# Kernel tuning notes

Measured on AMD Instinct MI355X. Metric: run time of the kernel, lower is better.

## Reference

```python
import jax, jax.numpy as jnp
import numpy as np

NUM_UNITS = 64
IN_FEATURES = 256
OUT_FEATURES = 256


def _uw(x, w):
    # per-unit linear: x [B,U,I], w [U,I,O] -> [B,U,O]
    return jnp.einsum('bui,uio->buo', x, w)


def setup_inputs() -> dict:
    key = jax.random.key(0)
    ks = jax.random.split(key, 8)
    bound = float(np.sqrt(1.0 / OUT_FEATURES))
    U, I, O = NUM_UNITS, IN_FEATURES, OUT_FEATURES
    B = 256
    uni = lambda k, s: jax.random.uniform(k, s, jnp.float32, -bound, bound)
    return {
        'x': jax.random.normal(ks[0], (B, U, I), jnp.float32),
        'w_ir': uni(ks[1], (U, I, O)),
        'w_iz': uni(ks[2], (U, I, O)),
        'w_in': uni(ks[3], (U, I, O)),
        'w_hr': uni(ks[4], (U, O, O)),
        'w_hz': uni(ks[5], (U, O, O)),
        'w_hn': uni(ks[6], (U, O, O)),
        'hidden_init': uni(ks[7], (1, U, O)),
    }


def reference(x, w_ir, w_iz, w_in, w_hr, w_hz, w_hn, hidden_init):
    # hidden initialized by broadcasting hidden_init over batch (first call)
    h = jnp.broadcast_to(hidden_init, (x.shape[0],) + hidden_init.shape[1:])
    r = jax.nn.sigmoid(_uw(x, w_ir) + _uw(h, w_hr))
    z = jax.nn.sigmoid(_uw(x, w_iz) + _uw(h, w_hz))
    n = jnp.tanh(_uw(x, w_in) + r * _uw(h, w_hn))
    return (1.0 - z) * n + z * h
```

## Files before the change

kernel.cpp:

```cpp
#include <hip/hip_runtime.h>

#define BATCH 256
#define UNITS 64
#define IFEAT 256
#define OFEAT 256

typedef __attribute__((ext_vector_type(8))) short v8s;
typedef __attribute__((ext_vector_type(4))) float v4f;

static __device__ __forceinline__ unsigned short f2bf(float f) {
    unsigned int x = __float_as_uint(f);
    unsigned int r = x + 0x7fffu + ((x >> 16) & 1u);
    return (unsigned short)(r >> 16);
}

static __device__ __forceinline__ float sigmoid_f(float x) {
    return 1.0f / (1.0f + __expf(-x));
}
static __device__ __forceinline__ float tanh_f(float x) {
    float ax = fabsf(x);
    float e = __expf(-2.0f * ax);
    float t = (1.0f - e) / (1.0f + e);
    return copysignf(t, x);
}

__global__ void gru_hvec(const float* __restrict__ whr,
                         const float* __restrict__ whz,
                         const float* __restrict__ whn,
                         const float* __restrict__ hinit,
                         float* __restrict__ hv) {
    __shared__ float red[256];
    const int bid  = blockIdx.x;
    const int half = bid & 1;
    const int u    = (bid >> 1) & 63;
    const int w    = bid >> 7;
    const float* wh = (w == 0) ? whr : (w == 1) ? whz : whn;

    const int t = threadIdx.x;
    const int o = half * 128 + (t & 127);
    const int c = t >> 7;
    const float* hp = hinit + u * IFEAT;
    const float* wp = wh + (size_t)u * IFEAT * OFEAT + o;

    float acc = 0.0f;
    const int i0 = c * 128;
#pragma unroll 8
    for (int i = 0; i < 128; ++i) {
        acc += hp[i0 + i] * wp[(size_t)(i0 + i) * OFEAT];
    }
    red[t] = acc;
    __syncthreads();
    if (c == 0) hv[((size_t)w * UNITS + u) * OFEAT + o] = red[t] + red[t + 128];
}

__global__ __launch_bounds__(256, 3) void gru_gemm(
    const float* __restrict__ x,
    const float* __restrict__ wir,
    const float* __restrict__ wiz,
    const float* __restrict__ win,
    const float* __restrict__ hinit,
    const float* __restrict__ hv,
    float* __restrict__ out) {
    __shared__ unsigned short As[2][4][64][8];
    __shared__ unsigned short Bs[2][3][4][64][8];

    const int bid = blockIdx.x;
    const int u   = (bid & 7) + 8 * ((bid >> 3) >> 4);
    const int rem = (bid >> 3) & 15;
    const int b0  = (rem >> 2) * 64;
    const int o0  = (rem & 3) * 64;

    const int t    = threadIdx.x;
    const int lane = t & 63;
    const int wave = t >> 6;
    const int wm   = wave >> 1;
    const int wn   = wave & 1;
    const int lg   = lane >> 4;
    const int lr   = lane & 15;

    const int srow = t & 63;
    const int skg  = t >> 6;

    const size_t a_gbase = (size_t)(b0 + srow) * (UNITS * IFEAT)
                         + (size_t)u * IFEAT + skg * 8;
    const size_t b_gbase = (size_t)u * (IFEAT * OFEAT)
                         + (size_t)(skg * 8) * OFEAT + o0 + srow;

    v4f ra0, ra1;
    float rb0[8], rb1[8], rb2[8];

    auto stage_load = [&](int kk) {
        const float* ap = x + a_gbase + kk * 32;
        ra0 = *(const v4f*)ap;
        ra1 = *(const v4f*)(ap + 4);
        const size_t bo = b_gbase + (size_t)kk * 32 * OFEAT;
#pragma unroll
        for (int j = 0; j < 8; ++j) rb0[j] = wir[bo + (size_t)j * OFEAT];
#pragma unroll
        for (int j = 0; j < 8; ++j) rb1[j] = wiz[bo + (size_t)j * OFEAT];
#pragma unroll
        for (int j = 0; j < 8; ++j) rb2[j] = win[bo + (size_t)j * OFEAT];
    };

    auto stage_write = [&](int bb) {
        v8s av;
        av[0] = (short)f2bf(ra0[0]); av[1] = (short)f2bf(ra0[1]);
        av[2] = (short)f2bf(ra0[2]); av[3] = (short)f2bf(ra0[3]);
        av[4] = (short)f2bf(ra1[0]); av[5] = (short)f2bf(ra1[1]);
        av[6] = (short)f2bf(ra1[2]); av[7] = (short)f2bf(ra1[3]);
        *(v8s*)&As[bb][skg][srow][0] = av;
        v8s bv0, bv1, bv2;
#pragma unroll
        for (int j = 0; j < 8; ++j) bv0[j] = (short)f2bf(rb0[j]);
#pragma unroll
        for (int j = 0; j < 8; ++j) bv1[j] = (short)f2bf(rb1[j]);
#pragma unroll
        for (int j = 0; j < 8; ++j) bv2[j] = (short)f2bf(rb2[j]);
        *(v8s*)&Bs[bb][0][skg][srow][0] = bv0;
        *(v8s*)&Bs[bb][1][skg][srow][0] = bv1;
        *(v8s*)&Bs[bb][2][skg][srow][0] = bv2;
    };

    v4f acc[3][2][2];
#pragma unroll
    for (int g = 0; g < 3; ++g)
#pragma unroll
        for (int mi = 0; mi < 2; ++mi)
#pragma unroll
            for (int ni = 0; ni < 2; ++ni)
                acc[g][mi][ni] = (v4f){0.f, 0.f, 0.f, 0.f};

    stage_load(0);
    stage_write(0);
    stage_load(1);
    __syncthreads();

#pragma unroll 2
    for (int kk = 0; kk < 8; ++kk) {
        const int bb = kk & 1;
        if (kk < 7) stage_write(bb ^ 1);
        if (kk < 6) stage_load(kk + 2);

        v8s a0 = *(const v8s*)&As[bb][lg][wm * 32 + lr][0];
        v8s a1 = *(const v8s*)&As[bb][lg][wm * 32 + 16 + lr][0];
#pragma unroll
        for (int g = 0; g < 3; ++g) {
#pragma unroll
            for (int ni = 0; ni < 2; ++ni) {
                v8s b = *(const v8s*)&Bs[bb][g][lg][wn * 32 + ni * 16 + lr][0];
                acc[g][0][ni] = __builtin_amdgcn_mfma_f32_16x16x32_bf16(a0, b, acc[g][0][ni], 0, 0, 0);
                acc[g][1][ni] = __builtin_amdgcn_mfma_f32_16x16x32_bf16(a1, b, acc[g][1][ni], 0, 0, 0);
            }
        }
        if (kk < 7) __syncthreads();
    }

    const int obase = o0 + wn * 32 + lr;
    float hrv[2], hzv[2], hnv[2], h0v[2];
#pragma unroll
    for (int ni = 0; ni < 2; ++ni) {
        const int o = obase + ni * 16;
        hrv[ni] = hv[(0 * UNITS + u) * OFEAT + o];
        hzv[ni] = hv[(1 * UNITS + u) * OFEAT + o];
        hnv[ni] = hv[(2 * UNITS + u) * OFEAT + o];
        h0v[ni] = hinit[u * OFEAT + o];
    }
    const int rbase = b0 + wm * 32 + lg * 4;
#pragma unroll
    for (int mi = 0; mi < 2; ++mi) {
#pragma unroll
        for (int ni = 0; ni < 2; ++ni) {
            const int o = obase + ni * 16;
#pragma unroll
            for (int jj = 0; jj < 4; ++jj) {
                const int row = rbase + mi * 16 + jj;
                const float r = sigmoid_f(acc[0][mi][ni][jj] + hrv[ni]);
                const float z = sigmoid_f(acc[1][mi][ni][jj] + hzv[ni]);
                const float n = tanh_f(acc[2][mi][ni][jj] + r * hnv[ni]);
                out[((size_t)row * UNITS + u) * OFEAT + o] = (1.0f - z) * n + z * h0v[ni];
            }
        }
    }
}

extern "C" void kernel_launch(void* const* d_in, const int* in_sizes, int n_in,
                              void* d_out, int out_size, void* d_ws, size_t ws_size,
                              hipStream_t stream) {
    const float* x     = (const float*)d_in[0];
    const float* w_ir  = (const float*)d_in[1];
    const float* w_iz  = (const float*)d_in[2];
    const float* w_in  = (const float*)d_in[3];
    const float* w_hr  = (const float*)d_in[4];
    const float* w_hz  = (const float*)d_in[5];
    const float* w_hn  = (const float*)d_in[6];
    const float* hinit = (const float*)d_in[7];
    float* out = (float*)d_out;
    float* hv  = (float*)d_ws;

    gru_hvec<<<dim3(384), dim3(256), 0, stream>>>(w_hr, w_hz, w_hn, hinit, hv);
    gru_gemm<<<dim3(1024), dim3(256), 0, stream>>>(x, w_ir, w_iz, w_in, hinit, hv, out);
}
```

Before: 36.98 us.

## Halve GEMM output tile width and split hvec reduction four ways

The main GEMM now uses a 64x32 output tile per block instead of 64x64. That doubles the grid to 2048 blocks, halves the accumulator registers, and redistributes B-tile loads across threads, with the launch bound raised to 6 blocks per SM. The hidden-vector kernel runs 512 threads, each doing a quarter of the K reduction, for more parallelism. The risk is that each x tile is now loaded and converted twice, once per output half, which adds redundant A traffic and bf16 conversion.

Measured after the change: 43.34 us. +17.2%, slower.

```diff
diff --git a/kernel.cpp b/kernel.cpp
--- a/kernel.cpp
+++ b/kernel.cpp
@@ -24,12 +24,13 @@
     return copysignf(t, x);
 }
 
-__global__ void gru_hvec(const float* __restrict__ whr,
-                         const float* __restrict__ whz,
-                         const float* __restrict__ whn,
-                         const float* __restrict__ hinit,
-                         float* __restrict__ hv) {
-    __shared__ float red[256];
+__global__ __launch_bounds__(512, 8) void gru_hvec(
+        const float* __restrict__ whr,
+        const float* __restrict__ whz,
+        const float* __restrict__ whn,
+        const float* __restrict__ hinit,
+        float* __restrict__ hv) {
+    __shared__ float red[512];
     const int bid  = blockIdx.x;
     const int half = bid & 1;
     const int u    = (bid >> 1) & 63;
@@ -43,17 +44,19 @@
     const float* wp = wh + (size_t)u * IFEAT * OFEAT + o;
 
     float acc = 0.0f;
-    const int i0 = c * 128;
+    const int i0 = c * 64;
 #pragma unroll 8
-    for (int i = 0; i < 128; ++i) {
+    for (int i = 0; i < 64; ++i) {
         acc += hp[i0 + i] * wp[(size_t)(i0 + i) * OFEAT];
     }
     red[t] = acc;
     __syncthreads();
-    if (c == 0) hv[((size_t)w * UNITS + u) * OFEAT + o] = red[t] + red[t + 128];
+    if (c == 0)
+        hv[((size_t)w * UNITS + u) * OFEAT + o] =
+            red[t] + red[t + 128] + red[t + 256] + red[t + 384];
 }
 
-__global__ __launch_bounds__(256, 3) void gru_gemm(
+__global__ __launch_bounds__(256, 6) void gru_gemm(
     const float* __restrict__ x,
     const float* __restrict__ wir,
     const float* __restrict__ wiz,
@@ -62,13 +65,13 @@
     const float* __restrict__ hv,
     float* __restrict__ out) {
     __shared__ unsigned short As[2][4][64][8];
-    __shared__ unsigned short Bs[2][3][4][64][8];
+    __shared__ unsigned short Bs[2][3][4][32][8];
 
     const int bid = blockIdx.x;
-    const int u   = (bid & 7) + 8 * ((bid >> 3) >> 4);
-    const int rem = (bid >> 3) & 15;
-    const int b0  = (rem >> 2) * 64;
-    const int o0  = (rem & 3) * 64;
+    const int u   = (bid & 7) + 8 * (bid >> 8);
+    const int rem = (bid >> 3) & 31;
+    const int b0  = (rem >> 3) * 64;
+    const int o0  = (rem & 7) * 32;
 
     const int t    = threadIdx.x;
     const int lane = t & 63;
@@ -78,28 +81,34 @@
     const int lg   = lane >> 4;
     const int lr   = lane & 15;
 
-    const int srow = t & 63;
-    const int skg  = t >> 6;
+    const int arow = t & 63;
+    const int akg  = t >> 6;
+    const int a_gbase = (b0 + arow) * (UNITS * IFEAT) + u * IFEAT + akg * 8;
 
-    const size_t a_gbase = (size_t)(b0 + srow) * (UNITS * IFEAT)
-                         + (size_t)u * IFEAT + skg * 8;
-    const size_t b_gbase = (size_t)u * (IFEAT * OFEAT)
-                         + (size_t)(skg * 8) * OFEAT + o0 + srow;
+    const int it0 = t;
+    const int c0  = it0 & 31, kg0 = (it0 >> 5) & 3, g0 = it0 >> 7;
+    const float* wp0 = (g0 == 0) ? wir : wiz;
+    const bool has1 = (t < 128);
+    const int it1 = 256 + t;
+    const int c1  = it1 & 31, kg1 = (it1 >> 5) & 3;
+    const int bg0 = u * (IFEAT * OFEAT) + (kg0 * 8) * OFEAT + o0 + c0;
+    const int bg1 = u * (IFEAT * OFEAT) + (kg1 * 8) * OFEAT + o0 + c1;
 
     v4f ra0, ra1;
-    float rb0[8], rb1[8], rb2[8];
+    float rb0[8], rb1[8];
 
     auto stage_load = [&](int kk) {
         const float* ap = x + a_gbase + kk * 32;
         ra0 = *(const v4f*)ap;
         ra1 = *(const v4f*)(ap + 4);
-        const size_t bo = b_gbase + (size_t)kk * 32 * OFEAT;
+        const int off0 = bg0 + kk * 32 * OFEAT;
 #pragma unroll
-        for (int j = 0; j < 8; ++j) rb0[j] = wir[bo + (size_t)j * OFEAT];
+        for (int j = 0; j < 8; ++j) rb0[j] = wp0[off0 + j * OFEAT];
+        if (has1) {
+            const int off1 = bg1 + kk * 32 * OFEAT;
 #pragma unroll
-        for (int j = 0; j < 8; ++j) rb1[j] = wiz[bo + (size_t)j * OFEAT];
-#pragma unroll
-        for (int j = 0; j < 8; ++j) rb2[j] = win[bo + (size_t)j * OFEAT];
+            for (int j = 0; j < 8; ++j) rb1[j] = win[off1 + j * OFEAT];
+        }
     };
 
     auto stage_write = [&](int bb) {
@@ -108,27 +117,25 @@
         av[2] = (short)f2bf(ra0[2]); av[3] = (short)f2bf(ra0[3]);
         av[4] = (short)f2bf(ra1[0]); av[5] = (short)f2bf(ra1[1]);
         av[6] = (short)f2bf(ra1[2]); av[7] = (short)f2bf(ra1[3]);
-        *(v8s*)&As[bb][skg][srow][0] = av;
-        v8s bv0, bv1, bv2;
+        *(v8s*)&As[bb][akg][arow][0] = av;
+        v8s bv0;
 #pragma unroll
         for (int j = 0; j < 8; ++j) bv0[j] = (short)f2bf(rb0[j]);
+        *(v8s*)&Bs[bb][g0][kg0][c0][0] = bv0;
+        if (has1) {
+            v8s bv1;
 #pragma unroll
-        for (int j = 0; j < 8; ++j) bv1[j] = (short)f2bf(rb1[j]);
-#pragma unroll
-        for (int j = 0; j < 8; ++j) bv2[j] = (short)f2bf(rb2[j]);
-        *(v8s*)&Bs[bb][0][skg][srow][0] = bv0;
-        *(v8s*)&Bs[bb][1][skg][srow][0] = bv1;
-        *(v8s*)&Bs[bb][2][skg][srow][0] = bv2;
+            for (int j = 0; j < 8; ++j) bv1[j] = (short)f2bf(rb1[j]);
+            *(v8s*)&Bs[bb][2][kg1][c1][0] = bv1;
+        }
     };
 
-    v4f acc[3][2][2];
+    v4f acc[3][2];
 #pragma unroll
     for (int g = 0; g < 3; ++g)
 #pragma unroll
         for (int mi = 0; mi < 2; ++mi)
-#pragma unroll
-            for (int ni = 0; ni < 2; ++ni)
-                acc[g][mi][ni] = (v4f){0.f, 0.f, 0.f, 0.f};
+            acc[g][mi] = (v4f){0.f, 0.f, 0.f, 0.f};
 
     stage_load(0);
     stage_write(0);
@@ -145,40 +152,28 @@
         v8s a1 = *(const v8s*)&As[bb][lg][wm * 32 + 16 + lr][0];
 #pragma unroll
         for (int g = 0; g < 3; ++g) {
-#pragma unroll
-            for (int ni = 0; ni < 2; ++ni) {
-                v8s b = *(const v8s*)&Bs[bb][g][lg][wn * 32 + ni * 16 + lr][0];
-                acc[g][0][ni] = __builtin_amdgcn_mfma_f32_16x16x32_bf16(a0, b, acc[g][0][ni], 0, 0, 0);
-                acc[g][1][ni] = __builtin_amdgcn_mfma_f32_16x16x32_bf16(a1, b, acc[g][1][ni], 0, 0, 0);
-            }
+            v8s b = *(const v8s*)&Bs[bb][g][lg][wn * 16 + lr][0];
+            acc[g][0] = __builtin_amdgcn_mfma_f32_16x16x32_bf16(a0, b, acc[g][0], 0, 0, 0);
+            acc[g][1] = __builtin_amdgcn_mfma_f32_16x16x32_bf16(a1, b, acc[g][1], 0, 0, 0);
         }
         if (kk < 7) __syncthreads();
     }
 
-    const int obase = o0 + wn * 32 + lr;
-    float hrv[2], hzv[2], hnv[2], h0v[2];
-#pragma unroll
-    for (int ni = 0; ni < 2; ++ni) {
-        const int o = obase + ni * 16;
-        hrv[ni] = hv[(0 * UNITS + u) * OFEAT + o];
-        hzv[ni] = hv[(1 * UNITS + u) * OFEAT + o];
-        hnv[ni] = hv[(2 * UNITS + u) * OFEAT + o];
-        h0v[ni] = hinit[u * OFEAT + o];
-    }
+    const int o = o0 + wn * 16 + lr;
+    const float hrv = hv[(0 * UNITS + u) * OFEAT + o];
+    const float hzv = hv[(1 * UNITS + u) * OFEAT + o];
+    const float hnv = hv[(2 * UNITS + u) * OFEAT + o];
+    const float h0v = hinit[u * OFEAT + o];
     const int rbase = b0 + wm * 32 + lg * 4;
 #pragma unroll
     for (int mi = 0; mi < 2; ++mi) {
 #pragma unroll
-        for (int ni = 0; ni < 2; ++ni) {
-            const int o = obase + ni * 16;
-#pragma unroll
-            for (int jj = 0; jj < 4; ++jj) {
-                const int row = rbase + mi * 16 + jj;
-                const float r = sigmoid_f(acc[0][mi][ni][jj] + hrv[ni]);
-                const float z = sigmoid_f(acc[1][mi][ni][jj] + hzv[ni]);
-                const float n = tanh_f(acc[2][mi][ni][jj] + r * hnv[ni]);
-                out[((size_t)row * UNITS + u) * OFEAT + o] = (1.0f - z) * n + z * h0v[ni];
-            }
+        for (int jj = 0; jj < 4; ++jj) {
+            const int row = rbase + mi * 16 + jj;
+            const float r = sigmoid_f(acc[0][mi][jj] + hrv);
+            const float z = sigmoid_f(acc[1][mi][jj] + hzv);
+            const float n = tanh_f(acc[2][mi][jj] + r * hnv);
+            out[(row * UNITS + u) * OFEAT + o] = (1.0f - z) * n + z * h0v;
         }
     }
 }
@@ -197,6 +192,6 @@
     float* out = (float*)d_out;
     float* hv  = (float*)d_ws;
 
-    gru_hvec<<<dim3(384), dim3(256), 0, stream>>>(w_hr, w_hz, w_hn, hinit, hv);
-    gru_gemm<<<dim3(1024), dim3(256), 0, stream>>>(x, w_ir, w_iz, w_in, hinit, hv, out);
+    gru_hvec<<<dim3(384), dim3(512), 0, stream>>>(w_hr, w_hz, w_hn, hinit, hv);
+    gru_gemm<<<dim3(2048), dim3(256), 0, stream>>>(x, w_ir, w_iz, w_in, hinit, hv, out);
 }
```

## Widen GEMM tile to 64x128 with full A tile preloaded into LDS

Applied to the files above, without the earlier changes.

The gate GEMM kernel now uses 512-thread blocks covering 64 batch rows by 128 outputs, which halves the grid and doubles reuse of each weight tile. The whole 64x256 bf16 A tile is loaded into LDS once, in a row-skewed layout to avoid bank conflicts, while only B stays double-buffered. The hidden-vector kernel splits its reduction four ways across 512 threads. LDS usage per block grows substantially, which can reduce occupancy, and index arithmetic moves to 32-bit ints.

New measurement: 40.61 us. 9.8% more time.

```diff
diff --git a/kernel.cpp b/kernel.cpp
--- a/kernel.cpp
+++ b/kernel.cpp
@@ -24,12 +24,13 @@
     return copysignf(t, x);
 }
 
-__global__ void gru_hvec(const float* __restrict__ whr,
-                         const float* __restrict__ whz,
-                         const float* __restrict__ whn,
-                         const float* __restrict__ hinit,
-                         float* __restrict__ hv) {
-    __shared__ float red[256];
+__global__ __launch_bounds__(512, 8) void gru_hvec(
+        const float* __restrict__ whr,
+        const float* __restrict__ whz,
+        const float* __restrict__ whn,
+        const float* __restrict__ hinit,
+        float* __restrict__ hv) {
+    __shared__ float red[512];
     const int bid  = blockIdx.x;
     const int half = bid & 1;
     const int u    = (bid >> 1) & 63;
@@ -43,17 +44,19 @@
     const float* wp = wh + (size_t)u * IFEAT * OFEAT + o;
 
     float acc = 0.0f;
-    const int i0 = c * 128;
+    const int i0 = c * 64;
 #pragma unroll 8
-    for (int i = 0; i < 128; ++i) {
+    for (int i = 0; i < 64; ++i) {
         acc += hp[i0 + i] * wp[(size_t)(i0 + i) * OFEAT];
     }
     red[t] = acc;
     __syncthreads();
-    if (c == 0) hv[((size_t)w * UNITS + u) * OFEAT + o] = red[t] + red[t + 128];
-}
-
-__global__ __launch_bounds__(256, 3) void gru_gemm(
+    if (c == 0)
+        hv[((size_t)w * UNITS + u) * OFEAT + o] =
+            red[t] + red[t + 128] + red[t + 256] + red[t + 384];
+}
+
+__global__ __launch_bounds__(512, 4) void gru_gemm(
     const float* __restrict__ x,
     const float* __restrict__ wir,
     const float* __restrict__ wiz,
@@ -61,64 +64,50 @@
     const float* __restrict__ hinit,
     const float* __restrict__ hv,
     float* __restrict__ out) {
-    __shared__ unsigned short As[2][4][64][8];
-    __shared__ unsigned short Bs[2][3][4][64][8];
+    __shared__ unsigned short As[32][64][8];
+    __shared__ unsigned short Bs[2][3][4][128][8];
 
     const int bid = blockIdx.x;
-    const int u   = (bid & 7) + 8 * ((bid >> 3) >> 4);
-    const int rem = (bid >> 3) & 15;
-    const int b0  = (rem >> 2) * 64;
-    const int o0  = (rem & 3) * 64;
+    const int u   = (bid & 7) * 8 + (bid >> 6);
+    const int k6  = (bid >> 3) & 7;
+    const int b0  = (k6 >> 1) * 64;
+    const int o0  = (k6 & 1) * 128;
 
     const int t    = threadIdx.x;
     const int lane = t & 63;
     const int wave = t >> 6;
-    const int wm   = wave >> 1;
-    const int wn   = wave & 1;
+    const int wm   = wave >> 2;
+    const int wn   = wave & 3;
     const int lg   = lane >> 4;
     const int lr   = lane & 15;
 
-    const int srow = t & 63;
-    const int skg  = t >> 6;
-
-    const size_t a_gbase = (size_t)(b0 + srow) * (UNITS * IFEAT)
-                         + (size_t)u * IFEAT + skg * 8;
-    const size_t b_gbase = (size_t)u * (IFEAT * OFEAT)
-                         + (size_t)(skg * 8) * OFEAT + o0 + srow;
-
-    v4f ra0, ra1;
+    const int bcol = t & 127;
+    const int bkg  = t >> 7;
+    const int b_gbase = u * (IFEAT * OFEAT) + bkg * 8 * OFEAT + o0 + bcol;
+
     float rb0[8], rb1[8], rb2[8];
 
-    auto stage_load = [&](int kk) {
-        const float* ap = x + a_gbase + kk * 32;
-        ra0 = *(const v4f*)ap;
-        ra1 = *(const v4f*)(ap + 4);
-        const size_t bo = b_gbase + (size_t)kk * 32 * OFEAT;
-#pragma unroll
-        for (int j = 0; j < 8; ++j) rb0[j] = wir[bo + (size_t)j * OFEAT];
-#pragma unroll
-        for (int j = 0; j < 8; ++j) rb1[j] = wiz[bo + (size_t)j * OFEAT];
-#pragma unroll
-        for (int j = 0; j < 8; ++j) rb2[j] = win[bo + (size_t)j * OFEAT];
+    auto bload = [&](int kk) {
+        const int off = b_gbase + kk * 32 * OFEAT;
+#pragma unroll
+        for (int j = 0; j < 8; ++j) rb0[j] = wir[off + j * OFEAT];
+#pragma unroll
+        for (int j = 0; j < 8; ++j) rb1[j] = wiz[off + j * OFEAT];
+#pragma unroll
+        for (int j = 0; j < 8; ++j) rb2[j] = win[off + j * OFEAT];
     };
 
-    auto stage_write = [&](int bb) {
-        v8s av;
-        av[0] = (short)f2bf(ra0[0]); av[1] = (short)f2bf(ra0[1]);
-        av[2] = (short)f2bf(ra0[2]); av[3] = (short)f2bf(ra0[3]);
-        av[4] = (short)f2bf(ra1[0]); av[5] = (short)f2bf(ra1[1]);
-        av[6] = (short)f2bf(ra1[2]); av[7] = (short)f2bf(ra1[3]);
-        *(v8s*)&As[bb][skg][srow][0] = av;
-        v8s bv0, bv1, bv2;
-#pragma unroll
-        for (int j = 0; j < 8; ++j) bv0[j] = (short)f2bf(rb0[j]);
-#pragma unroll
-        for (int j = 0; j < 8; ++j) bv1[j] = (short)f2bf(rb1[j]);
-#pragma unroll
-        for (int j = 0; j < 8; ++j) bv2[j] = (short)f2bf(rb2[j]);
-        *(v8s*)&Bs[bb][0][skg][srow][0] = bv0;
-        *(v8s*)&Bs[bb][1][skg][srow][0] = bv1;
-        *(v8s*)&Bs[bb][2][skg][srow][0] = bv2;
+    auto bwrite = [&](int bb) {
+        v8s v0, v1, v2;
+#pragma unroll
+        for (int j = 0; j < 8; ++j) v0[j] = (short)f2bf(rb0[j]);
+#pragma unroll
+        for (int j = 0; j < 8; ++j) v1[j] = (short)f2bf(rb1[j]);
+#pragma unroll
+        for (int j = 0; j < 8; ++j) v2[j] = (short)f2bf(rb2[j]);
+        *(v8s*)&Bs[bb][0][bkg][bcol][0] = v0;
+        *(v8s*)&Bs[bb][1][bkg][bcol][0] = v1;
+        *(v8s*)&Bs[bb][2][bkg][bcol][0] = v2;
     };
 
     v4f acc[3][2][2];
@@ -130,19 +119,37 @@
             for (int ni = 0; ni < 2; ++ni)
                 acc[g][mi][ni] = (v4f){0.f, 0.f, 0.f, 0.f};
 
-    stage_load(0);
-    stage_write(0);
-    stage_load(1);
+    bload(0);
+    {
+        const int kq   = t & 31;
+        const int rsub = t >> 5;
+#pragma unroll
+        for (int c = 0; c < 4; ++c) {
+            const int row = c * 16 + rsub;
+            const float* ap = x + (b0 + row) * (UNITS * IFEAT) + u * IFEAT + kq * 8;
+            v4f q0 = *(const v4f*)ap;
+            v4f q1 = *(const v4f*)(ap + 4);
+            v8s av;
+            av[0] = (short)f2bf(q0[0]); av[1] = (short)f2bf(q0[1]);
+            av[2] = (short)f2bf(q0[2]); av[3] = (short)f2bf(q0[3]);
+            av[4] = (short)f2bf(q1[0]); av[5] = (short)f2bf(q1[1]);
+            av[6] = (short)f2bf(q1[2]); av[7] = (short)f2bf(q1[3]);
+            *(v8s*)&As[kq][(row + kq) & 63][0] = av;
+        }
+    }
+    bwrite(0);
+    bload(1);
     __syncthreads();
 
-#pragma unroll 2
+#pragma unroll
     for (int kk = 0; kk < 8; ++kk) {
         const int bb = kk & 1;
-        if (kk < 7) stage_write(bb ^ 1);
-        if (kk < 6) stage_load(kk + 2);
-
-        v8s a0 = *(const v8s*)&As[bb][lg][wm * 32 + lr][0];
-        v8s a1 = *(const v8s*)&As[bb][lg][wm * 32 + 16 + lr][0];
+        if (kk < 7) bwrite(bb ^ 1);
+        if (kk < 6) bload(kk + 2);
+
+        const int kq0 = kk * 4 + lg;
+        v8s a0 = *(const v8s*)&As[kq0][((wm * 32 + lr) + kq0) & 63][0];
+        v8s a1 = *(const v8s*)&As[kq0][((wm * 32 + 16 + lr) + kq0) & 63][0];
 #pragma unroll
         for (int g = 0; g < 3; ++g) {
 #pragma unroll
@@ -177,7 +184,7 @@
                 const float r = sigmoid_f(acc[0][mi][ni][jj] + hrv[ni]);
                 const float z = sigmoid_f(acc[1][mi][ni][jj] + hzv[ni]);
                 const float n = tanh_f(acc[2][mi][ni][jj] + r * hnv[ni]);
-                out[((size_t)row * UNITS + u) * OFEAT + o] = (1.0f - z) * n + z * h0v[ni];
+                out[(row * UNITS + u) * OFEAT + o] = (1.0f - z) * n + z * h0v[ni];
             }
         }
     }
@@ -197,6 +204,6 @@
     float* out = (float*)d_out;
     float* hv  = (float*)d_ws;
 
-    gru_hvec<<<dim3(384), dim3(256), 0, stream>>>(w_hr, w_hz, w_hn, hinit, hv);
-    gru_gemm<<<dim3(1024), dim3(256), 0, stream>>>(x, w_ir, w_iz, w_in, hinit, hv, out);
-}
+    gru_hvec<<<dim3(384), dim3(512), 0, stream>>>(w_hr, w_hz, w_hn, hinit, hv);
+    gru_gemm<<<dim3(512), dim3(512), 0, stream>>>(x, w_ir, w_iz, w_in, hinit, hv, out);
+}
```
